# Kernel tuning notes

Hardware: AMD Instinct MI355X
Metric: run time of the kernel (lower is better)

Reference implementation:

```python
import jax, jax.numpy as jnp
import numpy as np

B, S, D = 2, 2048, 2048
H = 1024          # per-expert swiglu hidden
E = 16            # num_experts
K = 2             # top_k
T = B * S
CAP = (K * T) // E  # capacity = top_k * tokens / experts * capacity_factor(1.0) = 512


def setup_inputs() -> dict:
    key = jax.random.key(0)
    ks = jax.random.split(key, 10)
    s = 0.02
    return {
        "hidden_states": jax.random.normal(ks[0], (B, S, D), jnp.float32),
        "gate_w": jax.random.normal(ks[1], (D, E), jnp.float32) * s,
        "w1": jax.random.normal(ks[2], (E, D, H), jnp.float32) * s,
        "w3": jax.random.normal(ks[3], (E, D, H), jnp.float32) * s,
        "w2": jax.random.normal(ks[4], (E, H, D), jnp.float32) * s,
        "sw1": jax.random.normal(ks[5], (D, H), jnp.float32) * s,
        "sw3": jax.random.normal(ks[6], (D, H), jnp.float32) * s,
        "sw2": jax.random.normal(ks[7], (H, D), jnp.float32) * s,
        "coef_w": jax.random.normal(ks[8], (D, 2), jnp.float32) * s,
        "coef_b": jnp.zeros((2,), jnp.float32),
    }


def _topk_gating(logits):
    """GShard-style top-k capacity gating. logits: [T,E] (gate runs in fp32).
    Returns combine [T,E,C], dispatch [T,E,C], l_aux scalar, exp_counts [E]."""
    probs = jax.nn.softmax(logits, axis=-1)                     # [T,E]
    top_vals, top_idx = jax.lax.top_k(probs, K)                 # [T,K]
    gates = top_vals / jnp.sum(top_vals, -1, keepdims=True)     # renormalize top-k
    masks = jax.nn.one_hot(top_idx, E, dtype=probs.dtype)       # [T,K,E]

    prior = jnp.zeros((E,), probs.dtype)
    combine = jnp.zeros((T, E, CAP), probs.dtype)
    for kk in range(K):  # fixed tiny K, structurally distinct slots
        m = masks[:, kk]                                        # [T,E]
        loc = jnp.cumsum(m, axis=0) - m + prior                 # position in expert buffer
        prior = prior + jnp.sum(m, axis=0)
        keep = m * (loc < CAP)                                  # capacity drop
        pos = jnp.sum(loc * m, axis=1).astype(jnp.int32)        # [T]
        loc_oh = jax.nn.one_hot(pos, CAP, dtype=probs.dtype)    # [T,C]
        combine = combine + gates[:, kk, None, None] * keep[:, :, None] * loc_oh[:, None, :]
    dispatch = (combine > 0).astype(probs.dtype)

    # load-balancing aux loss over top-1 assignment (GShard/DeepSpeed convention)
    me = jnp.mean(probs, axis=0)                                # [E]
    ce = jnp.mean(masks[:, 0], axis=0)                          # [E]
    l_aux = jnp.sum(me * ce) * E
    exp_counts = jnp.sum(masks, axis=(0, 1)).astype(jnp.int32)  # tokens routed per expert
    return combine, dispatch, l_aux, exp_counts


def _swiglu(x, a, b, c):
    return (jax.nn.silu(x @ a) * (x @ b)) @ c


def reference(hidden_states, gate_w, w1, w3, w2, sw1, sw3, sw2, coef_w, coef_b):
    x = hidden_states.reshape(T, D)
    logits = (x.astype(jnp.float32) @ gate_w)                   # gate kept in fp32
    combine, dispatch, l_aux, exp_counts = _topk_gating(logits)

    # dispatch -> grouped expert swiglu -> combine
    xe = jnp.einsum('tec,td->ecd', dispatch.astype(x.dtype), x)         # [E,C,D]
    h = jax.nn.silu(jnp.einsum('ecd,edh->ech', xe, w1)) * jnp.einsum('ecd,edh->ech', xe, w3)
    ye = jnp.einsum('ech,ehd->ecd', h, w2)                              # [E,C,D]
    moe_out = jnp.einsum('tec,ecd->td', combine.astype(x.dtype), ye)    # [T,D]

    # shared-expert residual MLP + softmax coefficient combine
    mlp_out = _swiglu(x, sw1, sw3, sw2)                                 # [T,D]
    coef = jax.nn.softmax(x @ coef_w + coef_b, axis=-1)                 # [T,2]
    out = moe_out * coef[:, 0:1] + mlp_out * coef[:, 1:2]
    return out.reshape(B, S, D), l_aux, exp_counts
```

## Files before the change

kernel.cpp:

```cpp
#include <hip/hip_runtime.h>
#include <hip/hip_bf16.h>
#include <stdint.h>

#define T_TOK 4096
#define DIM   2048
#define HID   1024
#define NE    16
#define CAPE  512

typedef __bf16 bf16x8 __attribute__((ext_vector_type(8)));
typedef float  f32x4  __attribute__((ext_vector_type(4)));

__device__ __forceinline__ ushort f2bf(float f) {
    union { float f; uint32_t u; } v; v.f = f;
    uint32_t r = (v.u + 0x7FFFu + ((v.u >> 16) & 1u)) >> 16;
    return (ushort)r;
}
__device__ __forceinline__ float bf2f(ushort u) {
    union { uint32_t u; float f; } v; v.u = (uint32_t)u << 16; return v.f;
}
__device__ __forceinline__ void gload16(const void* g, void* lds) {
    __builtin_amdgcn_global_load_lds(
        (const __attribute__((address_space(1))) uint32_t*)g,
        (__attribute__((address_space(3))) uint32_t*)lds, 16, 0, 0);
}
#define VMCNT(n) asm volatile("s_waitcnt vmcnt(" #n ")" ::: "memory")

__global__ __launch_bounds__(256) void logits_kernel(
    const float* __restrict__ x, const float* __restrict__ gate_w,
    const float* __restrict__ coef_w, float* __restrict__ logits,
    ushort* __restrict__ xb)
{
    int t = blockIdx.x * 4 + (threadIdx.x >> 6);
    int lane = threadIdx.x & 63;
    const float* xr = x + (size_t)t * DIM;
    float acc[18];
#pragma unroll
    for (int o = 0; o < 18; ++o) acc[o] = 0.f;
#pragma unroll
    for (int g = 0; g < DIM / 512; ++g) {
        int d = g * 512 + lane * 8;
        float4 a = *(const float4*)(xr + d);
        float4 b4 = *(const float4*)(xr + d + 4);
        float xv[8] = {a.x, a.y, a.z, a.w, b4.x, b4.y, b4.z, b4.w};
        ushort ob[8];
#pragma unroll
        for (int j = 0; j < 8; ++j) {
            const float* gw = gate_w + (size_t)(d + j) * NE;
#pragma unroll
            for (int o = 0; o < NE; ++o) acc[o] += xv[j] * gw[o];
            acc[16] += xv[j] * coef_w[(d + j) * 2 + 0];
            acc[17] += xv[j] * coef_w[(d + j) * 2 + 1];
            ob[j] = f2bf(xv[j]);
        }
        *(uint4*)(xb + (size_t)t * DIM + d) = *(uint4*)ob;
    }
#pragma unroll
    for (int off = 32; off > 0; off >>= 1) {
#pragma unroll
        for (int o = 0; o < 18; ++o) acc[o] += __shfl_down(acc[o], off, 64);
    }
    if (lane == 0) {
#pragma unroll
        for (int o = 0; o < 18; ++o) logits[(size_t)t * 18 + o] = acc[o];
    }
}

__global__ __launch_bounds__(256) void finish_kernel(
    const float* __restrict__ logits, const float* __restrict__ coef_b,
    int* __restrict__ topidx, float* __restrict__ gatesw,
    float* __restrict__ coefo, float* __restrict__ probs_part,
    float* __restrict__ laux)
{
    __shared__ float wred[4][NE];
    int t = blockIdx.x * 256 + threadIdx.x;
    float lg[18];
#pragma unroll
    for (int o = 0; o < 18; ++o) lg[o] = logits[(size_t)t * 18 + o];
    float p[NE];
    float m = lg[0];
#pragma unroll
    for (int e = 1; e < NE; ++e) m = fmaxf(m, lg[e]);
    float ssum = 0.f;
#pragma unroll
    for (int e = 0; e < NE; ++e) { p[e] = expf(lg[e] - m); ssum += p[e]; }
    float inv = 1.f / ssum;
#pragma unroll
    for (int e = 0; e < NE; ++e) p[e] *= inv;
    int i1 = 0;
#pragma unroll
    for (int e = 1; e < NE; ++e) if (p[e] > p[i1]) i1 = e;
    int i2 = -1;
#pragma unroll
    for (int e = 0; e < NE; ++e) { if (e == i1) continue; if (i2 < 0 || p[e] > p[i2]) i2 = e; }
    float g0 = p[i1], g1 = p[i2], gs = g0 + g1;
    topidx[t * 2 + 0] = i1; topidx[t * 2 + 1] = i2;
    gatesw[t * 2 + 0] = g0 / gs; gatesw[t * 2 + 1] = g1 / gs;
    float c0 = lg[16] + coef_b[0], c1 = lg[17] + coef_b[1];
    float cm = fmaxf(c0, c1);
    float e0 = expf(c0 - cm), e1 = expf(c1 - cm);
    float cs = e0 + e1;
    coefo[t * 2 + 0] = e0 / cs; coefo[t * 2 + 1] = e1 / cs;

    float r[NE];
#pragma unroll
    for (int e = 0; e < NE; ++e) r[e] = p[e];
#pragma unroll
    for (int off = 32; off > 0; off >>= 1) {
#pragma unroll
        for (int e = 0; e < NE; ++e) r[e] += __shfl_down(r[e], off, 64);
    }
    int wv = threadIdx.x >> 6, ln = threadIdx.x & 63;
    if (ln == 0) {
#pragma unroll
        for (int e = 0; e < NE; ++e) wred[wv][e] = r[e];
    }
    __syncthreads();
    if (threadIdx.x < NE)
        probs_part[blockIdx.x * NE + threadIdx.x] =
            wred[0][threadIdx.x] + wred[1][threadIdx.x]
          + wred[2][threadIdx.x] + wred[3][threadIdx.x];
    if (blockIdx.x == 0 && threadIdx.x == 0) laux[0] = 0.f;
}

__global__ __launch_bounds__(256) void scan_transpose(
    const int* __restrict__ topidx, const float* __restrict__ gatesw,
    const float* __restrict__ probs_part,
    int* __restrict__ sidx, float* __restrict__ swt,
    int* __restrict__ assign_token, int* __restrict__ nvalid,
    float* __restrict__ out_tail,
    const float* __restrict__ sw2, ushort* __restrict__ sw2T)
{
    __shared__ __align__(16) ushort tile[128][264];
    int tid = threadIdx.x;

    if (blockIdx.x < NE) {
        __shared__ int wcnt[4];
        __shared__ float fred[4];
        __shared__ int runs;
        __shared__ int cnt0s;
        int e = blockIdx.x;
        int wv = tid >> 6, ln = tid & 63;
        unsigned long long ltmask = (1ull << ln) - 1ull;
        if (tid == 0) runs = 0;
        __syncthreads();
        for (int kk = 0; kk < 2; ++kk) {
            for (int c = 0; c < T_TOK; c += 256) {
                int t = c + tid;
                bool m = (topidx[t * 2 + kk] == e);
                unsigned long long b = __ballot(m);
                int within = __popcll(b & ltmask);
                if (ln == 0) wcnt[wv] = __popcll(b);
                __syncthreads();
                int cross = 0;
                for (int w = 0; w < wv; ++w) cross += wcnt[w];
                int pos = runs + cross + within;
                if (m) {
                    bool keep = pos < CAPE;
                    sidx[t * 2 + kk] = keep ? (e * CAPE + pos) : -1;
                    swt[t * 2 + kk] = keep ? gatesw[t * 2 + kk] : 0.f;
                    if (keep) assign_token[e * CAPE + pos] = t;
                }
                __syncthreads();
                if (tid == 0) runs += wcnt[0] + wcnt[1] + wcnt[2] + wcnt[3];
                __syncthreads();
            }
            if (kk == 0 && tid == 0) cnt0s = runs;
            __syncthreads();
        }
        for (int p = runs + tid; p < CAPE; p += 256)
            assign_token[e * CAPE + p] = 0;
        float val = (tid < 16) ? probs_part[tid * NE + e] : 0.f;
#pragma unroll
        for (int off = 32; off > 0; off >>= 1) val += __shfl_down(val, off, 64);
        if (ln == 0) fred[wv] = val;
        __syncthreads();
        if (tid == 0) {
            float psum = fred[0] + fred[1] + fred[2] + fred[3];
            int total = runs;
            nvalid[e] = min(CAPE, total);
            out_tail[1 + e] = (float)total;
            float term = (psum / (float)T_TOK) * ((float)cnt0s / (float)T_TOK) * (float)NE;
            atomicAdd(&out_tail[0], term);
        }
        return;
    }

    int id = blockIdx.x - NE;
    int R = HID, C = DIM;
    int tx = id & 3, ty = id >> 2;
    const float* in = sw2;
    ushort* outp = sw2T;
    int r0 = tx * 256, c0 = ty * 128;
    int t31 = tid & 31, t8 = tid >> 5;

#pragma unroll
    for (int it = 0; it < 8; ++it) {
        int r4 = (it * 8 + t8) * 4;
        int c4 = t31 * 4;
        const float* ip = in + (size_t)(r0 + r4) * C + c0 + c4;
        float va[4][4];
        *(float4*)va[0] = *(const float4*)(ip);
        *(float4*)va[1] = *(const float4*)(ip + C);
        *(float4*)va[2] = *(const float4*)(ip + 2 * (size_t)C);
        *(float4*)va[3] = *(const float4*)(ip + 3 * (size_t)C);
#pragma unroll
        for (int j = 0; j < 4; ++j) {
            uint2 u;
            u.x = (uint32_t)f2bf(va[0][j]) | ((uint32_t)f2bf(va[1][j]) << 16);
            u.y = (uint32_t)f2bf(va[2][j]) | ((uint32_t)f2bf(va[3][j]) << 16);
            *(uint2*)&tile[c4 + j][r4] = u;
        }
    }
    __syncthreads();

#pragma unroll
    for (int it = 0; it < 16; ++it) {
        int c = it * 8 + t8;
        int k = t31 * 8;
        uint4 o = *(const uint4*)&tile[c][k];
        *(uint4*)(outp + (size_t)(c0 + c) * R + r0 + k) = o;
    }
}

__device__ __forceinline__ void stage_half_off(
    const ushort* __restrict__ G, int k0, char* region, int tid,
    size_t off0, size_t off1)
{
#pragma unroll
    for (int q = 0; q < 2; ++q) {
        int c = q * 512 + tid;
        int row = c >> 3;
        int cb = (c & 7) << 4;
        int scb = cb ^ ((row & 7) << 4);
        const ushort* src = G + (q ? off1 : off0) + k0 + (scb >> 1);
        gload16(src, region + ((c - (tid & 63)) << 4));
    }
}

__device__ __forceinline__ bf16x8 ldfrag(const char* lds, int region, int row, int cb) {
    return *(const bf16x8*)(lds + region + row * 128 + (cb ^ ((row & 7) << 4)));
}

template<int NB>
__device__ __forceinline__ void core_single(
    const ushort* __restrict__ A, const ushort* __restrict__ B,
    size_t a0, size_t a1, size_t a2, size_t a3,
    size_t b0, size_t b1, size_t b2, size_t b3,
    int K, char* lds, f32x4 (&acc)[8][NB], int tid)
{
    const int DB = 32768 + NB * 8192;
    int lane = tid & 63;
    int wid = tid >> 6;
    int wrow = wid >> 2, wcol = wid & 3;
    int l15 = lane & 15, hi = lane >> 4;

#pragma unroll
    for (int m = 0; m < 8; ++m)
#pragma unroll
        for (int n = 0; n < NB; ++n)
            acc[m][n] = (f32x4){0.f, 0.f, 0.f, 0.f};

    int nj = K >> 7;

    stage_half_off(A, 0, lds + 0,           tid, a0, a1);
    stage_half_off(A, 0, lds + 16384,       tid, a2, a3);
    stage_half_off(B, 0, lds + 32768,       tid, b0, b1);
    if (NB == 4) stage_half_off(B, 0, lds + 32768 + 16384, tid, b2, b3);
    stage_half_off(B, 64, lds + DB + 32768, tid, b0, b1);
    if (NB == 4) stage_half_off(B, 64, lds + DB + 32768 + 16384, tid, b2, b3);
    if (NB == 4) VMCNT(4); else VMCNT(2);
    __builtin_amdgcn_s_barrier();
    __builtin_amdgcn_sched_barrier(0);

    for (int j = 0; j < nj; ++j) {
        int k1 = (2 * j + 1) << 6, k2 = (2 * j + 2) << 6, k3 = (2 * j + 3) << 6;
        bool st = (j < nj - 1);
#pragma unroll
        for (int d = 0; d < 2; ++d) {
            char* LA = lds + d * DB;
            char* LB = LA + 32768;
            char* LAo = lds + (d ^ 1) * DB;
            bf16x8 bf[NB][2];
#pragma unroll
            for (int p = 0; p < 4; ++p) {
                if (p == 0) {
#pragma unroll
                    for (int n = 0; n < NB; ++n)
#pragma unroll
                        for (int ks = 0; ks < 2; ++ks)
                            bf[n][ks] = ldfrag(LB, 0, wcol * (16 * NB) + n * 16 + l15, ks * 64 + hi * 16);
                }
                bf16x8 af[2][2];
#pragma unroll
                for (int i = 0; i < 2; ++i)
#pragma unroll
                    for (int ks = 0; ks < 2; ++ks)
                        af[i][ks] = ldfrag(LA, 0, wrow * 128 + (2 * p + i) * 16 + l15, ks * 64 + hi * 16);
                if (d == 0) {
                    if (p == 0)      stage_half_off(A, k1, LAo,         tid, a0, a1);
                    else if (p == 1) stage_half_off(A, k1, LAo + 16384, tid, a2, a3);
                    else if (p == 2) { if (st) stage_half_off(B, k2, LB, tid, b0, b1); }
                    else             { if (st && NB == 4) stage_half_off(B, k2, LB + 16384, tid, b2, b3); }
                } else {
                    if (st) {
                        if (p == 0)      stage_half_off(A, k2, LAo,         tid, a0, a1);
                        else if (p == 1) stage_half_off(A, k2, LAo + 16384, tid, a2, a3);
                        else if (p == 2) stage_half_off(B, k3, LB, tid, b0, b1);
                        else             { if (NB == 4) stage_half_off(B, k3, LB + 16384, tid, b2, b3); }
                    }
                }
                __builtin_amdgcn_s_barrier();
                if (p == 3) {
                    if (d == 0) {
                        if (st) { if (NB == 4) VMCNT(4); else VMCNT(2); }
                        else    VMCNT(0);
                    } else if (st) {
                        if (NB == 4) VMCNT(4); else VMCNT(2);
                    }
                }
                asm volatile("s_waitcnt lgkmcnt(0)" ::: "memory");
                __builtin_amdgcn_sched_barrier(0);
                __builtin_amdgcn_s_setprio(1);
#pragma unroll
                for (int i = 0; i < 2; ++i)
#pragma unroll
                    for (int n = 0; n < NB; ++n)
#pragma unroll
                        for (int ks = 0; ks < 2; ++ks)
                            acc[2 * p + i][n] = __builtin_amdgcn_mfma_f32_16x16x32_bf16(
                                af[i][ks], bf[n][ks], acc[2 * p + i][n], 0, 0, 0);
                __builtin_amdgcn_s_setprio(0);
                __builtin_amdgcn_s_barrier();
                __builtin_amdgcn_sched_barrier(0);
            }
        }
    }
}

__global__ __launch_bounds__(512, 2) void gemm2_up(
    const ushort* __restrict__ xb,
    const float* __restrict__ w1f, const float* __restrict__ w3f,
    const float* __restrict__ sw1f, const float* __restrict__ sw3f,
    const int* __restrict__ assign_token,
    ushort* __restrict__ HH, const int* __restrict__ nvalid)
{
    __shared__ __align__(16) char lds[131072];
    int b = blockIdx.x;
    int tid = threadIdx.x;
    int rr = tid >> 3;
    int lane = tid & 63, wid = tid >> 6;
    int wrow = wid >> 2, wcol = wid & 3;
    int l15 = lane & 15, hi = lane >> 4;

    if (b < 256) {
        int id = (b & 7) * 32 + (b >> 3);
        int e = id >> 4, rem = id & 15;
        int mt = rem >> 3, nt = rem & 7;
        int bm = mt * 256, bn = nt * 128;
        if (bm >= nvalid[e]) return;
        const int* at = assign_token + e * CAPE + bm;
        size_t a0 = (size_t)at[rr] * DIM;
        size_t a1 = (size_t)at[64 + rr] * DIM;
        size_t a2 = (size_t)at[128 + rr] * DIM;
        size_t a3 = (size_t)at[192 + rr] * DIM;
        int nq = tid & 63;
        int kb = (tid >> 6) * 8;
        const float* Wsrc = (nq < 32)
            ? (w1f + (size_t)e * DIM * HID + bn + nq * 4)
            : (w3f + (size_t)e * DIM * HID + bn + (nq - 32) * 4);

        f32x4 acc1[8][2], acc3[8][2];
#pragma unroll
        for (int m = 0; m < 8; ++m)
#pragma unroll
            for (int n = 0; n < 2; ++n) {
                acc1[m][n] = (f32x4){0.f, 0.f, 0.f, 0.f};
                acc3[m][n] = (f32x4){0.f, 0.f, 0.f, 0.f};
            }

        float4 breg[8];
        stage_half_off(xb, 0, lds + 0,     tid, a0, a1);
        stage_half_off(xb, 0, lds + 16384, tid, a2, a3);
        {
            const float* src = Wsrc + (size_t)kb * HID;
#pragma unroll
            for (int kk = 0; kk < 8; ++kk)
                breg[kk] = *(const float4*)(src + (size_t)kk * HID);
        }
        {
            char* LB = lds + 32768;
#pragma unroll
            for (int j = 0; j < 4; ++j) {
                int r = nq * 4 + j;
                ushort pk[8];
#pragma unroll
                for (int kk = 0; kk < 8; ++kk) pk[kk] = f2bf(((const float*)&breg[kk])[j]);
                int cb = (kb * 2) ^ ((r & 7) << 4);
                *(uint4*)(LB + r * 128 + cb) = *(uint4*)pk;
            }
        }
        VMCNT(0);
        __syncthreads();

        int d = 0;
        for (int t = 0; t < DIM / 64; ++t) {
            bool pf = (t < DIM / 64 - 1);
            char* LA = lds + d * 65536;
            char* LB = LA + 32768;
            char* LAo = lds + (d ^ 1) * 65536;
            char* LBo = LAo + 32768;
            if (pf) {
                int k0 = (t + 1) * 64;
                stage_half_off(xb, k0, LAo,         tid, a0, a1);
                stage_half_off(xb, k0, LAo + 16384, tid, a2, a3);
                const float* src = Wsrc + (size_t)(k0 + kb) * HID;
#pragma unroll
                for (int kk = 0; kk < 8; ++kk)
                    breg[kk] = *(const float4*)(src + (size_t)kk * HID);
            }
#pragma unroll
            for (int ks = 0; ks < 2; ++ks) {
                bf16x8 af[8], bf1[2], bf3[2];
#pragma unroll
                for (int m = 0; m < 8; ++m)
                    af[m] = ldfrag(LA, 0, wrow * 128 + m * 16 + l15, ks * 64 + hi * 16);
#pragma unroll
                for (int n = 0; n < 2; ++n) {
                    bf1[n] = ldfrag(LB, 0, wcol * 32 + n * 16 + l15,       ks * 64 + hi * 16);
                    bf3[n] = ldfrag(LB, 0, 128 + wcol * 32 + n * 16 + l15, ks * 64 + hi * 16);
                }
#pragma unroll
                for (int m = 0; m < 8; ++m)
#pragma unroll
                    for (int n = 0; n < 2; ++n) {
                        acc1[m][n] = __builtin_amdgcn_mfma_f32_16x16x32_bf16(
                            af[m], bf1[n], acc1[m][n], 0, 0, 0);
                        acc3[m][n] = __builtin_amdgcn_mfma_f32_16x16x32_bf16(
                            af[m], bf3[n], acc3[m][n], 0, 0, 0);
                    }
            }
            if (pf) {
#pragma unroll
                for (int j = 0; j < 4; ++j) {
                    int r = nq * 4 + j;
                    ushort pk[8];
#pragma unroll
                    for (int kk = 0; kk < 8; ++kk) pk[kk] = f2bf(((const float*)&breg[kk])[j]);
                    int cb = (kb * 2) ^ ((r & 7) << 4);
                    *(uint4*)(LBo + r * 128 + cb) = *(uint4*)pk;
                }
            }
            VMCNT(0);
            __syncthreads();
            d ^= 1;
        }

        ushort* O = HH + (size_t)e * CAPE * HID;
        int rbase = bm + wrow * 128 + (lane >> 4) * 4;
        int cbase = bn + wcol * 32 + (lane & 15);
#pragma unroll
        for (int m = 0; m < 8; ++m)
#pragma unroll
            for (int n = 0; n < 2; ++n) {
                int col = cbase + n * 16;
#pragma unroll
                for (int r = 0; r < 4; ++r) {
                    float g = acc1[m][n][r];
                    float s = g / (1.f + __expf(-g));
                    O[(size_t)(rbase + m * 16 + r) * HID + col] = f2bf(s * acc3[m][n][r]);
                }
            }
    } else {
        int b2 = b - 256;
        int id = (b2 & 7) * 32 + (b2 >> 3);
        int mt = id >> 4, nt = id & 15;
        int bm = mt * 256, bn = nt * 64;
        size_t a0 = (size_t)(bm + rr) * DIM;
        size_t a1 = (size_t)(bm + 64 + rr) * DIM;
        size_t a2 = (size_t)(bm + 128 + rr) * DIM;
        size_t a3 = (size_t)(bm + 192 + rr) * DIM;
        int nq = tid & 31;
        int kb = (tid >> 5) * 4;
        const float* Wsrc = (nq < 16)
            ? (sw1f + bn + nq * 4)
            : (sw3f + bn + (nq - 16) * 4);

        f32x4 acc1[8][1], acc3[8][1];
#pragma unroll
        for (int m = 0; m < 8; ++m) {
            acc1[m][0] = (f32x4){0.f, 0.f, 0.f, 0.f};
            acc3[m][0] = (f32x4){0.f, 0.f, 0.f, 0.f};
        }

        float4 breg[4];
        stage_half_off(xb, 0, lds + 0,     tid, a0, a1);
        stage_half_off(xb, 0, lds + 16384, tid, a2, a3);
        {
            const float* src = Wsrc + (size_t)kb * HID;
#pragma unroll
            for (int kk = 0; kk < 4; ++kk)
                breg[kk] = *(const float4*)(src + (size_t)kk * HID);
        }
        {
            char* LB = lds + 32768;
#pragma unroll
            for (int j = 0; j < 4; ++j) {
                int r = nq * 4 + j;
                ushort pk[4];
#pragma unroll
                for (int kk = 0; kk < 4; ++kk) pk[kk] = f2bf(((const float*)&breg[kk])[j]);
                int cb = (kb * 2) ^ ((r & 7) << 4);
                *(uint2*)(LB + r * 128 + cb) = *(uint2*)pk;
            }
        }
        VMCNT(0);
        __syncthreads();

        int d = 0;
        for (int t = 0; t < DIM / 64; ++t) {
            bool pf = (t < DIM / 64 - 1);
            char* LA = lds + d * 65536;
            char* LB = LA + 32768;
            char* LAo = lds + (d ^ 1) * 65536;
            char* LBo = LAo + 32768;
            if (pf) {
                int k0 = (t + 1) * 64;
                stage_half_off(xb, k0, LAo,         tid, a0, a1);
                stage_half_off(xb, k0, LAo + 16384, tid, a2, a3);
                const float* src = Wsrc + (size_t)(k0 + kb) * HID;
#pragma unroll
                for (int kk = 0; kk < 4; ++kk)
                    breg[kk] = *(const float4*)(src + (size_t)kk * HID);
            }
#pragma unroll
            for (int ks = 0; ks < 2; ++ks) {
                bf16x8 af[8], bf1, bf3;
#pragma unroll
                for (int m = 0; m < 8; ++m)
                    af[m] = ldfrag(LA, 0, wrow * 128 + m * 16 + l15, ks * 64 + hi * 16);
                bf1 = ldfrag(LB, 0, wcol * 16 + l15,      ks * 64 + hi * 16);
                bf3 = ldfrag(LB, 0, 64 + wcol * 16 + l15, ks * 64 + hi * 16);
#pragma unroll
                for (int m = 0; m < 8; ++m) {
                    acc1[m][0] = __builtin_amdgcn_mfma_f32_16x16x32_bf16(
                        af[m], bf1, acc1[m][0], 0, 0, 0);
                    acc3[m][0] = __builtin_amdgcn_mfma_f32_16x16x32_bf16(
                        af[m], bf3, acc3[m][0], 0, 0, 0);
                }
            }
            if (pf) {
#pragma unroll
                for (int j = 0; j < 4; ++j) {
                    int r = nq * 4 + j;
                    ushort pk[4];
#pragma unroll
                    for (int kk = 0; kk < 4; ++kk) pk[kk] = f2bf(((const float*)&breg[kk])[j]);
                    int cb = (kb * 2) ^ ((r & 7) << 4);
                    *(uint2*)(LBo + r * 128 + cb) = *(uint2*)pk;
                }
            }
            VMCNT(0);
            __syncthreads();
            d ^= 1;
        }

        ushort* O = HH + (size_t)NE * CAPE * HID;
        int rbase = bm + wrow * 128 + (lane >> 4) * 4;
        int col = bn + wcol * 16 + (lane & 15);
#pragma unroll
        for (int m = 0; m < 8; ++m)
#pragma unroll
            for (int r = 0; r < 4; ++r) {
                float g = acc1[m][0][r];
                float s = g / (1.f + __expf(-g));
                O[(size_t)(rbase + m * 16 + r) * HID + col] = f2bf(s * acc3[m][0][r]);
            }
    }
}

__global__ __launch_bounds__(512, 2) void gemm8_down(
    const ushort* __restrict__ HH, const float* __restrict__ w2f,
    const ushort* __restrict__ sw2T, ushort* __restrict__ ye,
    ushort* __restrict__ mlpb, const float* __restrict__ coefo,
    const int* __restrict__ nvalid)
{
    __shared__ __align__(16) char lds[131072];
    int b = blockIdx.x;
    int tid = threadIdx.x;
    int rr = tid >> 3;
    int lane = tid & 63, wid = tid >> 6;
    int wrow = wid >> 2, wcol = wid & 3;

    if (b < 256) {
        int id = (b & 7) * 32 + (b >> 3);
        int e = id >> 4, rem = id & 15;
        int mt = rem >> 3, nt = rem & 7;
        int bm = mt * 256, bn = nt * 256;
        if (bm >= nvalid[e]) return;
        const ushort* A = HH + (size_t)e * CAPE * HID;
        const float*  W = w2f + (size_t)e * HID * DIM;
        ushort* Ob = ye + (size_t)e * CAPE * DIM;
        size_t a0 = (size_t)(bm + rr) * HID;
        size_t a1 = (size_t)(bm + 64 + rr) * HID;
        size_t a2 = (size_t)(bm + 128 + rr) * HID;
        size_t a3 = (size_t)(bm + 192 + rr) * HID;
        int nq = tid & 63;
        int kb = (tid >> 6) * 8;
        int l15 = lane & 15, hi = lane >> 4;

        f32x4 acc[8][4];
#pragma unroll
        for (int m = 0; m < 8; ++m)
#pragma unroll
            for (int n = 0; n < 4; ++n)
                acc[m][n] = (f32x4){0.f, 0.f, 0.f, 0.f};

        float4 breg[8];
        stage_half_off(A, 0, lds + 0,     tid, a0, a1);
        stage_half_off(A, 0, lds + 16384, tid, a2, a3);
        {
            const float* src = W + (size_t)kb * DIM + bn + nq * 4;
#pragma unroll
            for (int kk = 0; kk < 8; ++kk)
                breg[kk] = *(const float4*)(src + (size_t)kk * DIM);
        }
        {
            char* LB = lds + 32768;
#pragma unroll
            for (int j = 0; j < 4; ++j) {
                int r = nq * 4 + j;
                ushort pk[8];
#pragma unroll
                for (int kk = 0; kk < 8; ++kk) pk[kk] = f2bf(((const float*)&breg[kk])[j]);
                int cb = (kb * 2) ^ ((r & 7) << 4);
                *(uint4*)(LB + r * 128 + cb) = *(uint4*)pk;
            }
        }
        VMCNT(0);
        __syncthreads();

        int d = 0;
        for (int t = 0; t < HID / 64; ++t) {
            bool pf = (t < HID / 64 - 1);
            char* LA = lds + d * 65536;
            char* LB = LA + 32768;
            char* LAo = lds + (d ^ 1) * 65536;
            char* LBo = LAo + 32768;
            if (pf) {
                int k0 = (t + 1) * 64;
                stage_half_off(A, k0, LAo,         tid, a0, a1);
                stage_half_off(A, k0, LAo + 16384, tid, a2, a3);
                const float* src = W + (size_t)(k0 + kb) * DIM + bn + nq * 4;
#pragma unroll
                for (int kk = 0; kk < 8; ++kk)
                    breg[kk] = *(const float4*)(src + (size_t)kk * DIM);
            }
#pragma unroll
            for (int ks = 0; ks < 2; ++ks) {
                bf16x8 af[8], bf[4];
#pragma unroll
                for (int m = 0; m < 8; ++m)
                    af[m] = ldfrag(LA, 0, wrow * 128 + m * 16 + l15, ks * 64 + hi * 16);
#pragma unroll
                for (int n = 0; n < 4; ++n)
                    bf[n] = ldfrag(LB, 0, wcol * 64 + n * 16 + l15, ks * 64 + hi * 16);
#pragma unroll
                for (int m = 0; m < 8; ++m)
#pragma unroll
                    for (int n = 0; n < 4; ++n)
                        acc[m][n] = __builtin_amdgcn_mfma_f32_16x16x32_bf16(
                            af[m], bf[n], acc[m][n], 0, 0, 0);
            }
            if (pf) {
#pragma unroll
                for (int j = 0; j < 4; ++j) {
                    int r = nq * 4 + j;
                    ushort pk[8];
#pragma unroll
                    for (int kk = 0; kk < 8; ++kk) pk[kk] = f2bf(((const float*)&breg[kk])[j]);
                    int cb = (kb * 2) ^ ((r & 7) << 4);
                    *(uint4*)(LBo + r * 128 + cb) = *(uint4*)pk;
                }
            }
            VMCNT(0);
            __syncthreads();
            d ^= 1;
        }

        int rbase = bm + wrow * 128 + (lane >> 4) * 4;
        int cbase = bn + wcol * 64 + (lane & 15);
#pragma unroll
        for (int m = 0; m < 8; ++m)
#pragma unroll
            for (int n = 0; n < 4; ++n) {
                int col = cbase + n * 16;
#pragma unroll
                for (int r = 0; r < 4; ++r)
                    Ob[(size_t)(rbase + m * 16 + r) * DIM + col] = f2bf(acc[m][n][r]);
            }
    } else {
        int b2i = b - 256;
        int id = (b2i & 7) * 32 + (b2i >> 3);
        int mt = id >> 4, nt = id & 15;
        int bm = mt * 256, bn = nt * 128;
        const ushort* A = HH + (size_t)NE * CAPE * HID;
        const ushort* B = sw2T;
        size_t a0 = (size_t)(bm + rr) * HID;
        size_t a1 = (size_t)(bm + 64 + rr) * HID;
        size_t a2 = (size_t)(bm + 128 + rr) * HID;
        size_t a3 = (size_t)(bm + 192 + rr) * HID;
        size_t b0 = (size_t)(bn + rr) * HID;
        size_t b1 = (size_t)(bn + 64 + rr) * HID;
        f32x4 acc[8][2];
        core_single<2>(A, B, a0, a1, a2, a3, b0, b1, 0, 0, HID, lds, acc, tid);
        int rbase = bm + wrow * 128 + (lane >> 4) * 4;
        int cbase = bn + wcol * 32 + (lane & 15);
#pragma unroll
        for (int m = 0; m < 8; ++m)
#pragma unroll
            for (int n = 0; n < 2; ++n) {
                int col = cbase + n * 16;
#pragma unroll
                for (int r = 0; r < 4; ++r) {
                    int row = rbase + m * 16 + r;
                    mlpb[(size_t)row * DIM + col] = f2bf(acc[m][n][r] * coefo[2 * row + 1]);
                }
            }
    }
}

__global__ __launch_bounds__(256) void combine_kernel(
    const ushort* __restrict__ ye, const ushort* __restrict__ mlpb,
    const int* __restrict__ sidx, const float* __restrict__ swt,
    const float* __restrict__ coefo, float* __restrict__ out)
{
    int idx = blockIdx.x * 256 + threadIdx.x;
    int t = idx >> 9;
    int d = (idx & 511) << 2;
    int s0 = sidx[t * 2], s1 = sidx[t * 2 + 1];
    float c0 = coefo[t * 2];
    float w0 = swt[t * 2] * c0, w1 = swt[t * 2 + 1] * c0;
    uint2 mb = *(const uint2*)(mlpb + (size_t)t * DIM + d);
    const ushort* mp = (const ushort*)&mb;
    float4 v;
    v.x = bf2f(mp[0]); v.y = bf2f(mp[1]); v.z = bf2f(mp[2]); v.w = bf2f(mp[3]);
    if (s0 >= 0) {
        uint2 y = *(const uint2*)(ye + (size_t)s0 * DIM + d);
        const ushort* yp = (const ushort*)&y;
        v.x += w0 * bf2f(yp[0]); v.y += w0 * bf2f(yp[1]);
        v.z += w0 * bf2f(yp[2]); v.w += w0 * bf2f(yp[3]);
    }
    if (s1 >= 0) {
        uint2 y = *(const uint2*)(ye + (size_t)s1 * DIM + d);
        const ushort* yp = (const ushort*)&y;
        v.x += w1 * bf2f(yp[0]); v.y += w1 * bf2f(yp[1]);
        v.z += w1 * bf2f(yp[2]); v.w += w1 * bf2f(yp[3]);
    }
    *(float4*)(out + (size_t)t * DIM + d) = v;
}

extern "C" void kernel_launch(void* const* d_in, const int* in_sizes, int n_in,
                              void* d_out, int out_size, void* d_ws, size_t ws_size,
                              hipStream_t stream)
{
    const float* x      = (const float*)d_in[0];
    const float* gate_w = (const float*)d_in[1];
    const float* w1     = (const float*)d_in[2];
    const float* w3     = (const float*)d_in[3];
    const float* w2     = (const float*)d_in[4];
    const float* sw1    = (const float*)d_in[5];
    const float* sw3    = (const float*)d_in[6];
    const float* sw2    = (const float*)d_in[7];
    const float* coef_w = (const float*)d_in[8];
    const float* coef_b = (const float*)d_in[9];
    float* out = (float*)d_out;

    char* ws = (char*)d_ws;
    size_t off = 0;
    auto alloc = [&](size_t bytes) -> void* {
        void* p = ws + off;
        off += (bytes + 255) & ~(size_t)255;
        return p;
    };
    int*    nvalid       = (int*)alloc(NE * 4);
    int*    topidx       = (int*)alloc((size_t)T_TOK * 2 * 4);
    float*  gatesw       = (float*)alloc((size_t)T_TOK * 2 * 4);
    float*  coefo        = (float*)alloc((size_t)T_TOK * 2 * 4);
    int*    sidx         = (int*)alloc((size_t)T_TOK * 2 * 4);
    float*  swt          = (float*)alloc((size_t)T_TOK * 2 * 4);
    int*    assign_token = (int*)alloc((size_t)NE * CAPE * 4);
    float*  probs_part   = (float*)alloc((size_t)16 * NE * 4);
    float*  logits       = (float*)alloc((size_t)T_TOK * 18 * 4);
    ushort* sw2T = (ushort*)alloc((size_t)DIM * HID * 2);
    ushort* xb   = (ushort*)alloc((size_t)T_TOK * DIM * 2);
    size_t HROWS = (size_t)NE * CAPE + T_TOK;
    ushort* HH   = (ushort*)alloc(HROWS * HID * 2);
    ushort* ye   = (ushort*)alloc((size_t)NE * CAPE * DIM * 2);
    ushort* mlpb = (ushort*)alloc((size_t)T_TOK * DIM * 2);

    float* out_tail = out + (size_t)T_TOK * DIM;

    logits_kernel<<<T_TOK / 4, 256, 0, stream>>>(x, gate_w, coef_w, logits, xb);
    finish_kernel<<<T_TOK / 256, 256, 0, stream>>>(logits, coef_b, topidx, gatesw,
                                                   coefo, probs_part, out_tail);
    scan_transpose<<<NE + 64, 256, 0, stream>>>(
        topidx, gatesw, probs_part, sidx, swt, assign_token, nvalid, out_tail,
        sw2, sw2T);
    gemm2_up<<<512, 512, 0, stream>>>(xb, w1, w3, sw1, sw3, assign_token, HH, nvalid);
    gemm8_down<<<512, 512, 0, stream>>>(HH, w2, sw2T, ye, mlpb, coefo, nvalid);
    combine_kernel<<<(T_TOK * (DIM / 4)) / 256, 256, 0, stream>>>(
        ye, mlpb, sidx, swt, coefo, out);
}
```

Measured before the change: 355.6 us.

## Relax vmcnt waits so global-to-LDS loads overlap MFMA compute

```diff
diff --git a/kernel.cpp b/kernel.cpp
--- a/kernel.cpp
+++ b/kernel.cpp
@@ -25,6 +25,7 @@
         (__attribute__((address_space(3))) uint32_t*)lds, 16, 0, 0);
 }
 #define VMCNT(n) asm volatile("s_waitcnt vmcnt(" #n ")" ::: "memory")
+#define LGKM0    asm volatile("s_waitcnt lgkmcnt(0)" ::: "memory")
 
 __global__ __launch_bounds__(256) void logits_kernel(
     const float* __restrict__ x, const float* __restrict__ gate_w,
@@ -380,15 +381,15 @@
             }
 
         float4 breg[8];
+        {
+            const float* src = Wsrc + (size_t)kb * HID;
+#pragma unroll
+            for (int kk = 0; kk < 8; ++kk)
+                breg[kk] = *(const float4*)(src + (size_t)kk * HID);
+        }
         stage_half_off(xb, 0, lds + 0,     tid, a0, a1);
         stage_half_off(xb, 0, lds + 16384, tid, a2, a3);
         {
-            const float* src = Wsrc + (size_t)kb * HID;
-#pragma unroll
-            for (int kk = 0; kk < 8; ++kk)
-                breg[kk] = *(const float4*)(src + (size_t)kk * HID);
-        }
-        {
             char* LB = lds + 32768;
 #pragma unroll
             for (int j = 0; j < 4; ++j) {
@@ -400,8 +401,9 @@
                 *(uint4*)(LB + r * 128 + cb) = *(uint4*)pk;
             }
         }
-        VMCNT(0);
-        __syncthreads();
+        LGKM0;
+        __builtin_amdgcn_sched_barrier(0);
+        __builtin_amdgcn_s_barrier();
 
         int d = 0;
         for (int t = 0; t < DIM / 64; ++t) {
@@ -412,13 +414,17 @@
             char* LBo = LAo + 32768;
             if (pf) {
                 int k0 = (t + 1) * 64;
+                const float* src = Wsrc + (size_t)(k0 + kb) * HID;
+#pragma unroll
+                for (int kk = 0; kk < 8; ++kk)
+                    breg[kk] = *(const float4*)(src + (size_t)kk * HID);
                 stage_half_off(xb, k0, LAo,         tid, a0, a1);
                 stage_half_off(xb, k0, LAo + 16384, tid, a2, a3);
-                const float* src = Wsrc + (size_t)(k0 + kb) * HID;
-#pragma unroll
-                for (int kk = 0; kk < 8; ++kk)
-                    breg[kk] = *(const float4*)(src + (size_t)kk * HID);
-            }
+                VMCNT(12);
+            } else {
+                VMCNT(0);
+            }
+            __builtin_amdgcn_sched_barrier(0);
 #pragma unroll
             for (int ks = 0; ks < 2; ++ks) {
                 bf16x8 af[8], bf1[2], bf3[2];
@@ -451,8 +457,9 @@
                     *(uint4*)(LBo + r * 128 + cb) = *(uint4*)pk;
                 }
             }
-            VMCNT(0);
-            __syncthreads();
+            LGKM0;
+            __builtin_amdgcn_sched_barrier(0);
+            __builtin_amdgcn_s_barrier();
             d ^= 1;
         }
 
@@ -494,15 +501,15 @@
         }
 
         float4 breg[4];
+        {
+            const float* src = Wsrc + (size_t)kb * HID;
+#pragma unroll
+            for (int kk = 0; kk < 4; ++kk)
+                breg[kk] = *(const float4*)(src + (size_t)kk * HID);
+        }
         stage_half_off(xb, 0, lds + 0,     tid, a0, a1);
         stage_half_off(xb, 0, lds + 16384, tid, a2, a3);
         {
-            const float* src = Wsrc + (size_t)kb * HID;
-#pragma unroll
-            for (int kk = 0; kk < 4; ++kk)
-                breg[kk] = *(const float4*)(src + (size_t)kk * HID);
-        }
-        {
             char* LB = lds + 32768;
 #pragma unroll
             for (int j = 0; j < 4; ++j) {
@@ -514,8 +521,9 @@
                 *(uint2*)(LB + r * 128 + cb) = *(uint2*)pk;
             }
         }
-        VMCNT(0);
-        __syncthreads();
+        LGKM0;
+        __builtin_amdgcn_sched_barrier(0);
+        __builtin_amdgcn_s_barrier();
 
         int d = 0;
         for (int t = 0; t < DIM / 64; ++t) {
@@ -526,13 +534,17 @@
             char* LBo = LAo + 32768;
             if (pf) {
                 int k0 = (t + 1) * 64;
+                const float* src = Wsrc + (size_t)(k0 + kb) * HID;
+#pragma unroll
+                for (int kk = 0; kk < 4; ++kk)
+                    breg[kk] = *(const float4*)(src + (size_t)kk * HID);
                 stage_half_off(xb, k0, LAo,         tid, a0, a1);
                 stage_half_off(xb, k0, LAo + 16384, tid, a2, a3);
-                const float* src = Wsrc + (size_t)(k0 + kb) * HID;
-#pragma unroll
-                for (int kk = 0; kk < 4; ++kk)
-                    breg[kk] = *(const float4*)(src + (size_t)kk * HID);
-            }
+                VMCNT(8);
+            } else {
+                VMCNT(0);
+            }
+            __builtin_amdgcn_sched_barrier(0);
 #pragma unroll
             for (int ks = 0; ks < 2; ++ks) {
                 bf16x8 af[8], bf1, bf3;
@@ -560,8 +572,9 @@
                     *(uint2*)(LBo + r * 128 + cb) = *(uint2*)pk;
                 }
             }
-            VMCNT(0);
-            __syncthreads();
+            LGKM0;
+            __builtin_amdgcn_sched_barrier(0);
+            __builtin_amdgcn_s_barrier();
             d ^= 1;
         }
 
@@ -617,15 +630,15 @@
                 acc[m][n] = (f32x4){0.f, 0.f, 0.f, 0.f};
 
         float4 breg[8];
+        {
+            const float* src = W + (size_t)kb * DIM + bn + nq * 4;
+#pragma unroll
+            for (int kk = 0; kk < 8; ++kk)
+                breg[kk] = *(const float4*)(src + (size_t)kk * DIM);
+        }
         stage_half_off(A, 0, lds + 0,     tid, a0, a1);
         stage_half_off(A, 0, lds + 16384, tid, a2, a3);
         {
-            const float* src = W + (size_t)kb * DIM + bn + nq * 4;
-#pragma unroll
-            for (int kk = 0; kk < 8; ++kk)
-                breg[kk] = *(const float4*)(src + (size_t)kk * DIM);
-        }
-        {
             char* LB = lds + 32768;
 #pragma unroll
             for (int j = 0; j < 4; ++j) {
@@ -637,8 +650,9 @@
                 *(uint4*)(LB + r * 128 + cb) = *(uint4*)pk;
             }
         }
-        VMCNT(0);
-        __syncthreads();
+        LGKM0;
+        __builtin_amdgcn_sched_barrier(0);
+        __builtin_amdgcn_s_barrier();
 
         int d = 0;
         for (int t = 0; t < HID / 64; ++t) {
@@ -649,13 +663,17 @@
             char* LBo = LAo + 32768;
             if (pf) {
                 int k0 = (t + 1) * 64;
+                const float* src = W + (size_t)(k0 + kb) * DIM + bn + nq * 4;
+#pragma unroll
+                for (int kk = 0; kk < 8; ++kk)
+                    breg[kk] = *(const float4*)(src + (size_t)kk * DIM);
                 stage_half_off(A, k0, LAo,         tid, a0, a1);
                 stage_half_off(A, k0, LAo + 16384, tid, a2, a3);
-                const float* src = W + (size_t)(k0 + kb) * DIM + bn + nq * 4;
-#pragma unroll
-                for (int kk = 0; kk < 8; ++kk)
-                    breg[kk] = *(const float4*)(src + (size_t)kk * DIM);
-            }
+                VMCNT(12);
+            } else {
+                VMCNT(0);
+            }
+            __builtin_amdgcn_sched_barrier(0);
 #pragma unroll
             for (int ks = 0; ks < 2; ++ks) {
                 bf16x8 af[8], bf[4];
@@ -683,8 +701,9 @@
                     *(uint4*)(LBo + r * 128 + cb) = *(uint4*)pk;
                 }
             }
-            VMCNT(0);
-            __syncthreads();
+            LGKM0;
+            __builtin_amdgcn_sched_barrier(0);
+            __builtin_amdgcn_s_barrier();
             d ^= 1;
         }
 
```

Result: slower. 369.4 us (+3.9%).
